# Optimization experiments

Measured on AMD Instinct MI355X. Metric: run time of the kernel, lower is better.

Reference implementation:

```python
import jax, jax.numpy as jnp
import numpy as np

NUM_NODES = 100000
DIM_E = 64
NEG_SLOPE = 0.01  # F.leaky_relu default


def setup_inputs() -> dict:
    key = jax.random.key(0)
    ks = jax.random.split(key, 8)
    edge_index = jax.random.randint(ks[0], (2, 1000000), 0, NUM_NODES, dtype=jnp.int64)
    # xavier_normal for id_embedding: std = sqrt(2/(fan_in+fan_out))
    std_emb = float(np.sqrt(2.0 / (NUM_NODES + DIM_E)))
    id_embedding = jax.random.normal(ks[1], (NUM_NODES, DIM_E), dtype=jnp.float32) * std_emb
    std_w = float(np.sqrt(2.0 / (DIM_E + DIM_E)))  # glorot for GCN lin weight [out, in]
    W1 = jax.random.normal(ks[2], (DIM_E, DIM_E), dtype=jnp.float32) * std_w
    W2 = jax.random.normal(ks[3], (DIM_E, DIM_E), dtype=jnp.float32) * std_w
    W3 = jax.random.normal(ks[4], (DIM_E, DIM_E), dtype=jnp.float32) * std_w
    b1 = jnp.zeros((DIM_E,), dtype=jnp.float32)
    b2 = jnp.zeros((DIM_E,), dtype=jnp.float32)
    b3 = jnp.zeros((DIM_E,), dtype=jnp.float32)
    return {"edge_index": edge_index, "id_embedding": id_embedding,
            "W1": W1, "b1": b1, "W2": W2, "b2": b2, "W3": W3, "b3": b3}


def _build_graph(edge_index, n):
    # symmetrize (as done in RealGCN.forward) then add self loops (PyG GCNConv default)
    ei = jnp.concatenate([edge_index, edge_index[::-1]], axis=1)
    loops = jnp.arange(n, dtype=ei.dtype)
    row = jnp.concatenate([ei[0], loops])  # source
    col = jnp.concatenate([ei[1], loops])  # destination
    deg = jax.ops.segment_sum(jnp.ones_like(col, dtype=jnp.float32), col, num_segments=n)
    dinv = jnp.where(deg > 0, jax.lax.rsqrt(deg), 0.0)
    norm = dinv[row] * dinv[col]  # [E_total]
    return row, col, norm


def _gcn_conv(x, row, col, norm, W, b, n):
    h = x @ W.T                                   # [N, D] linear transform
    msg = h[row] * norm[:, None]                  # gather + normalize
    out = jax.ops.segment_sum(msg, col, num_segments=n)  # scatter-add
    return out + b


def reference(edge_index, id_embedding, W1, b1, W2, b2, W3, b3):
    n = id_embedding.shape[0]
    row, col, norm = _build_graph(edge_index, n)
    # has_norm: L2-normalize rows (F.normalize, eps=1e-12)
    nrm = jnp.linalg.norm(id_embedding, axis=1, keepdims=True)
    x = id_embedding / jnp.maximum(nrm, 1e-12)
    x1 = jax.nn.leaky_relu(_gcn_conv(x, row, col, norm, W1, b1, n), NEG_SLOPE)
    x2 = jax.nn.leaky_relu(_gcn_conv(x1, row, col, norm, W2, b2, n), NEG_SLOPE)
    x3 = _gcn_conv(x1, row, col, norm, W3, b3, n)  # note: layer 3 has no activation
    return x + x1 + x2 + x3
```

## Files before the change

### kernel.cpp

```cpp
#include <hip/hip_runtime.h>
#include <math.h>

#define DIM 64
#define NEG_SLOPE 0.01f

typedef unsigned short bfraw;
typedef unsigned int uint32;

__device__ __forceinline__ bfraw f2bf(float f) {
    unsigned int u = __float_as_uint(f);
    unsigned int r = (u + 0x7FFFu + ((u >> 16) & 1u)) >> 16;
    return (bfraw)r;
}
__device__ __forceinline__ float bflo(uint32 u) { return __uint_as_float(u << 16); }
__device__ __forceinline__ float bfhi(uint32 u) { return __uint_as_float(u & 0xFFFF0000u); }
__device__ __forceinline__ uint32 pack2(float lo, float hi) {
    return (uint32)f2bf(lo) | ((uint32)f2bf(hi) << 16);
}

#define EPW 4096

__global__ __launch_bounds__(256) void k_bin(const int* __restrict__ ei, int E,
                                             uint32* __restrict__ stage,
                                             int* __restrict__ bcur, int shift, int sbits,
                                             int capS) {
    __shared__ int hist[256];
    __shared__ int cur[256];
    int t = threadIdx.x;
    hist[t] = 0;
    __syncthreads();
    int e0 = blockIdx.x * EPW;
    int e1 = e0 + EPW < E ? e0 + EPW : E;
    uint32 lmask = (1u << shift) - 1u;
    for (int e = e0 + t; e < e1; e += 256) {
        int u = ei[e], v = ei[E + e];
        atomicAdd(&hist[u >> shift], 1);
        atomicAdd(&hist[v >> shift], 1);
    }
    __syncthreads();
    cur[t] = hist[t] > 0 ? (t * capS + atomicAdd(&bcur[t * 16], hist[t])) : 0;
    __syncthreads();
    for (int e = e0 + t; e < e1; e += 256) {
        int u = ei[e], v = ei[E + e];
        int s1 = atomicAdd(&cur[v >> shift], 1);
        stage[s1] = (((uint32)v & lmask) << sbits) | (uint32)u;
        int s2 = atomicAdd(&cur[u >> shift], 1);
        stage[s2] = (((uint32)u & lmask) << sbits) | (uint32)v;
    }
}

__global__ __launch_bounds__(256) void k_bucket(const uint32* __restrict__ stage,
                                                const int* __restrict__ bcur,
                                                int* __restrict__ offsets,
                                                int* __restrict__ oend,
                                                int* __restrict__ adj,
                                                float* __restrict__ dinv,
                                                int n, int shift, int sbits,
                                                int capS, int capA) {
    __shared__ int deg[2048];
    __shared__ int scan[256];
    int t = threadIdx.x;
    int span  = 1 << shift;
    int node0 = blockIdx.x << shift;
    int cnt = n - node0 < span ? n - node0 : span;
    uint32 smask = (1u << sbits) - 1u;
    for (int i = t; i < cnt; i += 256) deg[i] = 0;
    __syncthreads();
    int jbeg = blockIdx.x * capS;
    int jend = jbeg + bcur[blockIdx.x * 16];
    for (int j = jbeg + t; j < jend; j += 256)
        atomicAdd(&deg[stage[j] >> sbits], 1);
    __syncthreads();
    int per  = span >> 8;
    int base = t * per;
    int s = 0;
    for (int k = 0; k < per; k++) { int i = base + k; if (i < cnt) s += deg[i] + 1; }
    scan[t] = s;
    __syncthreads();
    for (int off = 1; off < 256; off <<= 1) {
        int v = (t >= off) ? scan[t - off] : 0;
        __syncthreads();
        scan[t] += v;
        __syncthreads();
    }
    int run = blockIdx.x * capA + scan[t] - s;
    for (int k = 0; k < per; k++) {
        int i = base + k;
        if (i < cnt) {
            int d = deg[i];
            offsets[node0 + i] = run;
            oend[node0 + i]    = run + 1 + d;
            dinv[node0 + i] = rsqrtf(1.0f + (float)d);
            adj[run] = node0 + i;
            deg[i] = run + 1;
            run += d + 1;
        }
    }
    __syncthreads();
    for (int j = jbeg + t; j < jend; j += 256) {
        uint32 r = stage[j];
        int slot = atomicAdd(&deg[r >> sbits], 1);
        adj[slot] = (int)(r & smask);
    }
}

__global__ void k_normalize(const float* __restrict__ x, const float* __restrict__ dinv,
                            bfraw* __restrict__ xnb, bfraw* __restrict__ xnw, int n) {
    int row  = (blockIdx.x * blockDim.x + threadIdx.x) >> 6;
    int lane = threadIdx.x & 63;
    if (row >= n) return;
    float v = x[row * DIM + lane];
    float s = v * v;
    #pragma unroll
    for (int off = 32; off; off >>= 1) s += __shfl_xor(s, off);
    float scale = 1.0f / fmaxf(sqrtf(s), 1e-12f);
    float xv = v * scale;
    xnb[row * DIM + lane] = f2bf(xv);
    xnw[row * DIM + lane] = f2bf(xv * dinv[row]);
}

#define ACC8(p) { a0 += bflo(p.x); a1 += bfhi(p.x); a2 += bflo(p.y); a3 += bfhi(p.y); \
                  a4 += bflo(p.z); a5 += bfhi(p.z); a6 += bflo(p.w); a7 += bfhi(p.w); }

__global__ void k_gather(const int* __restrict__ adj, const int* __restrict__ offsets,
                         const int* __restrict__ oend,
                         const float* __restrict__ dinv,
                         const bfraw* __restrict__ srcw,
                         bfraw* __restrict__ dstb, int n) {
    int w    = (blockIdx.x * blockDim.x + threadIdx.x) >> 6;
    int lane = threadIdx.x & 63;
    if (w >= n) return;
    int oct = lane >> 3;
    int ol  = lane & 7;
    int beg = offsets[w], end = oend[w];
    float dd = dinv[w];
    const uint4* rows = (const uint4*)srcw;
    float a0 = 0.f, a1 = 0.f, a2 = 0.f, a3 = 0.f;
    float a4 = 0.f, a5 = 0.f, a6 = 0.f, a7 = 0.f;
    int j = beg;
    for (; j + 32 <= end; j += 32) {
        int s0 = adj[j + oct];
        int s1 = adj[j + 8 + oct];
        int s2 = adj[j + 16 + oct];
        int s3 = adj[j + 24 + oct];
        uint4 p0 = rows[(size_t)s0 * 8 + ol];
        uint4 p1 = rows[(size_t)s1 * 8 + ol];
        uint4 p2 = rows[(size_t)s2 * 8 + ol];
        uint4 p3 = rows[(size_t)s3 * 8 + ol];
        ACC8(p0) ACC8(p1) ACC8(p2) ACC8(p3)
    }
    if (j + 16 <= end) {
        int s0 = adj[j + oct];
        int s1 = adj[j + 8 + oct];
        uint4 p0 = rows[(size_t)s0 * 8 + ol];
        uint4 p1 = rows[(size_t)s1 * 8 + ol];
        ACC8(p0) ACC8(p1)
        j += 16;
    }
    if (j + 8 <= end) {
        int s0 = adj[j + oct];
        uint4 p0 = rows[(size_t)s0 * 8 + ol];
        ACC8(p0)
        j += 8;
    }
    int rem = end - j;
    if (oct < rem) {
        int s0 = adj[j + oct];
        uint4 p0 = rows[(size_t)s0 * 8 + ol];
        ACC8(p0)
    }
    a0 += __shfl_xor(a0, 8); a0 += __shfl_xor(a0, 16); a0 += __shfl_xor(a0, 32);
    a1 += __shfl_xor(a1, 8); a1 += __shfl_xor(a1, 16); a1 += __shfl_xor(a1, 32);
    a2 += __shfl_xor(a2, 8); a2 += __shfl_xor(a2, 16); a2 += __shfl_xor(a2, 32);
    a3 += __shfl_xor(a3, 8); a3 += __shfl_xor(a3, 16); a3 += __shfl_xor(a3, 32);
    a4 += __shfl_xor(a4, 8); a4 += __shfl_xor(a4, 16); a4 += __shfl_xor(a4, 32);
    a5 += __shfl_xor(a5, 8); a5 += __shfl_xor(a5, 16); a5 += __shfl_xor(a5, 32);
    a6 += __shfl_xor(a6, 8); a6 += __shfl_xor(a6, 16); a6 += __shfl_xor(a6, 32);
    a7 += __shfl_xor(a7, 8); a7 += __shfl_xor(a7, 16); a7 += __shfl_xor(a7, 32);
    if (lane < 8) {
        uint4 o;
        o.x = pack2(dd * a0, dd * a1);
        o.y = pack2(dd * a2, dd * a3);
        o.z = pack2(dd * a4, dd * a5);
        o.w = pack2(dd * a6, dd * a7);
        ((uint4*)(dstb + (size_t)w * DIM))[ol] = o;
    }
}


__global__ __launch_bounds__(256) void k_linear_rt(
    const bfraw* __restrict__ inb, const float* __restrict__ W,
    const float* __restrict__ b, const float* __restrict__ dinv,
    bfraw* __restrict__ outb, bfraw* __restrict__ outw, int n)
{
    __shared__ float  sIn[64][65];
    __shared__ uint32 sWp[64][32];
    int tid = threadIdx.x;
    int r0  = blockIdx.x * 64;
    #pragma unroll
    for (int i = 0; i < 8; i++) {
        int idx = tid + i * 256;
        int k = idx & 63, cp = idx >> 6;
        sWp[k][cp] = (uint32)f2bf(W[(2 * cp) * DIM + k]) |
                     ((uint32)f2bf(W[(2 * cp + 1) * DIM + k]) << 16);
    }
    int limu = ((n - r0 < 64 ? n - r0 : 64) * DIM) >> 1;
    const uint32* inu = (const uint32*)(inb + (size_t)r0 * DIM);
    for (int idx = tid; idx < limu; idx += 256) {
        uint32 u = inu[idx];
        int r = idx >> 5, c = (idx & 31) * 2;
        sIn[r][c] = bflo(u); sIn[r][c + 1] = bfhi(u);
    }
    __syncthreads();

    int ri = (tid >> 4) << 2;
    int ci = (tid & 15) << 2;
    int cp = ci >> 1;
    float acc[4][4];
    #pragma unroll
    for (int j = 0; j < 4; j++) {
        float bj = b[ci + j];
        #pragma unroll
        for (int i = 0; i < 4; i++) acc[i][j] = bj;
    }
    #pragma unroll 2
    for (int k4 = 0; k4 < 16; k4++) {
        int k = k4 * 4;
        float4 A0 = *(const float4*)&sIn[ri + 0][k];
        float4 A1 = *(const float4*)&sIn[ri + 1][k];
        float4 A2 = *(const float4*)&sIn[ri + 2][k];
        float4 A3 = *(const float4*)&sIn[ri + 3][k];
        #pragma unroll
        for (int kk = 0; kk < 4; kk++) {
            uint2 uw = *(const uint2*)&sWp[k + kk][cp];
            float w0 = bflo(uw.x), w1 = bfhi(uw.x);
            float w2 = bflo(uw.y), w3 = bfhi(uw.y);
            float a0 = kk == 0 ? A0.x : kk == 1 ? A0.y : kk == 2 ? A0.z : A0.w;
            float a1 = kk == 0 ? A1.x : kk == 1 ? A1.y : kk == 2 ? A1.z : A1.w;
            float a2 = kk == 0 ? A2.x : kk == 1 ? A2.y : kk == 2 ? A2.z : A2.w;
            float a3 = kk == 0 ? A3.x : kk == 1 ? A3.y : kk == 2 ? A3.z : A3.w;
            acc[0][0] = fmaf(a0, w0, acc[0][0]); acc[0][1] = fmaf(a0, w1, acc[0][1]);
            acc[0][2] = fmaf(a0, w2, acc[0][2]); acc[0][3] = fmaf(a0, w3, acc[0][3]);
            acc[1][0] = fmaf(a1, w0, acc[1][0]); acc[1][1] = fmaf(a1, w1, acc[1][1]);
            acc[1][2] = fmaf(a1, w2, acc[1][2]); acc[1][3] = fmaf(a1, w3, acc[1][3]);
            acc[2][0] = fmaf(a2, w0, acc[2][0]); acc[2][1] = fmaf(a2, w1, acc[2][1]);
            acc[2][2] = fmaf(a2, w2, acc[2][2]); acc[2][3] = fmaf(a2, w3, acc[2][3]);
            acc[3][0] = fmaf(a3, w0, acc[3][0]); acc[3][1] = fmaf(a3, w1, acc[3][1]);
            acc[3][2] = fmaf(a3, w2, acc[3][2]); acc[3][3] = fmaf(a3, w3, acc[3][3]);
        }
    }
    #pragma unroll
    for (int i = 0; i < 4; i++) {
        int r = r0 + ri + i;
        if (r >= n) break;
        float dd = dinv[r];
        float e0 = acc[i][0] > 0.f ? acc[i][0] : NEG_SLOPE * acc[i][0];
        float e1 = acc[i][1] > 0.f ? acc[i][1] : NEG_SLOPE * acc[i][1];
        float e2 = acc[i][2] > 0.f ? acc[i][2] : NEG_SLOPE * acc[i][2];
        float e3 = acc[i][3] > 0.f ? acc[i][3] : NEG_SLOPE * acc[i][3];
        ushort4 ob;
        ob.x = f2bf(e0); ob.y = f2bf(e1); ob.z = f2bf(e2); ob.w = f2bf(e3);
        *(ushort4*)&outb[(size_t)r * DIM + ci] = ob;
        ushort4 ow;
        ow.x = f2bf(e0 * dd); ow.y = f2bf(e1 * dd);
        ow.z = f2bf(e2 * dd); ow.w = f2bf(e3 * dd);
        *(ushort4*)&outw[(size_t)r * DIM + ci] = ow;
    }
}

__global__ __launch_bounds__(256) void k_final_rt(
    const bfraw* __restrict__ aggb, const bfraw* __restrict__ xnb,
    const bfraw* __restrict__ x1b,
    const float* __restrict__ W2, const float* __restrict__ b2,
    const float* __restrict__ W3, const float* __restrict__ b3,
    float* __restrict__ out, int n)
{
    __shared__ float  sIn[64][65];
    __shared__ uint32 sW2p[64][32];
    __shared__ uint32 sW3p[64][32];
    int tid = threadIdx.x;
    int r0  = blockIdx.x * 64;
    #pragma unroll
    for (int i = 0; i < 8; i++) {
        int idx = tid + i * 256;
        int k = idx & 63, cp = idx >> 6;
        sW2p[k][cp] = (uint32)f2bf(W2[(2 * cp) * DIM + k]) |
                      ((uint32)f2bf(W2[(2 * cp + 1) * DIM + k]) << 16);
        sW3p[k][cp] = (uint32)f2bf(W3[(2 * cp) * DIM + k]) |
                      ((uint32)f2bf(W3[(2 * cp + 1) * DIM + k]) << 16);
    }
    int limu = ((n - r0 < 64 ? n - r0 : 64) * DIM) >> 1;
    const uint32* inu = (const uint32*)(aggb + (size_t)r0 * DIM);
    for (int idx = tid; idx < limu; idx += 256) {
        uint32 u = inu[idx];
        int r = idx >> 5, c = (idx & 31) * 2;
        sIn[r][c] = bflo(u); sIn[r][c + 1] = bfhi(u);
    }
    __syncthreads();

    int ri = (tid >> 4) << 2;
    int ci = (tid & 15) << 2;
    int cp = ci >> 1;
    float acc2[4][4], acc3[4][4];
    #pragma unroll
    for (int j = 0; j < 4; j++) {
        float bj2 = b2[ci + j], bj3 = b3[ci + j];
        #pragma unroll
        for (int i = 0; i < 4; i++) { acc2[i][j] = bj2; acc3[i][j] = bj3; }
    }
    #pragma unroll 2
    for (int k4 = 0; k4 < 16; k4++) {
        int k = k4 * 4;
        float4 A0 = *(const float4*)&sIn[ri + 0][k];
        float4 A1 = *(const float4*)&sIn[ri + 1][k];
        float4 A2 = *(const float4*)&sIn[ri + 2][k];
        float4 A3 = *(const float4*)&sIn[ri + 3][k];
        #pragma unroll
        for (int kk = 0; kk < 4; kk++) {
            uint2 u2 = *(const uint2*)&sW2p[k + kk][cp];
            uint2 u3 = *(const uint2*)&sW3p[k + kk][cp];
            float a0 = kk == 0 ? A0.x : kk == 1 ? A0.y : kk == 2 ? A0.z : A0.w;
            float a1 = kk == 0 ? A1.x : kk == 1 ? A1.y : kk == 2 ? A1.z : A1.w;
            float a2 = kk == 0 ? A2.x : kk == 1 ? A2.y : kk == 2 ? A2.z : A2.w;
            float a3 = kk == 0 ? A3.x : kk == 1 ? A3.y : kk == 2 ? A3.z : A3.w;
            float u0 = bflo(u2.x), u1 = bfhi(u2.x), u2c = bflo(u2.y), u3c = bfhi(u2.y);
            float v0 = bflo(u3.x), v1 = bfhi(u3.x), v2c = bflo(u3.y), v3c = bfhi(u3.y);
            acc2[0][0] = fmaf(a0, u0, acc2[0][0]); acc2[0][1] = fmaf(a0, u1, acc2[0][1]);
            acc2[0][2] = fmaf(a0, u2c, acc2[0][2]); acc2[0][3] = fmaf(a0, u3c, acc2[0][3]);
            acc2[1][0] = fmaf(a1, u0, acc2[1][0]); acc2[1][1] = fmaf(a1, u1, acc2[1][1]);
            acc2[1][2] = fmaf(a1, u2c, acc2[1][2]); acc2[1][3] = fmaf(a1, u3c, acc2[1][3]);
            acc2[2][0] = fmaf(a2, u0, acc2[2][0]); acc2[2][1] = fmaf(a2, u1, acc2[2][1]);
            acc2[2][2] = fmaf(a2, u2c, acc2[2][2]); acc2[2][3] = fmaf(a2, u3c, acc2[2][3]);
            acc2[3][0] = fmaf(a3, u0, acc2[3][0]); acc2[3][1] = fmaf(a3, u1, acc2[3][1]);
            acc2[3][2] = fmaf(a3, u2c, acc2[3][2]); acc2[3][3] = fmaf(a3, u3c, acc2[3][3]);
            acc3[0][0] = fmaf(a0, v0, acc3[0][0]); acc3[0][1] = fmaf(a0, v1, acc3[0][1]);
            acc3[0][2] = fmaf(a0, v2c, acc3[0][2]); acc3[0][3] = fmaf(a0, v3c, acc3[0][3]);
            acc3[1][0] = fmaf(a1, v0, acc3[1][0]); acc3[1][1] = fmaf(a1, v1, acc3[1][1]);
            acc3[1][2] = fmaf(a1, v2c, acc3[1][2]); acc3[1][3] = fmaf(a1, v3c, acc3[1][3]);
            acc3[2][0] = fmaf(a2, v0, acc3[2][0]); acc3[2][1] = fmaf(a2, v1, acc3[2][1]);
            acc3[2][2] = fmaf(a2, v2c, acc3[2][2]); acc3[2][3] = fmaf(a2, v3c, acc3[2][3]);
            acc3[3][0] = fmaf(a3, v0, acc3[3][0]); acc3[3][1] = fmaf(a3, v1, acc3[3][1]);
            acc3[3][2] = fmaf(a3, v2c, acc3[3][2]); acc3[3][3] = fmaf(a3, v3c, acc3[3][3]);
        }
    }
    #pragma unroll
    for (int i = 0; i < 4; i++) {
        int r = r0 + ri + i;
        if (r >= n) break;
        size_t base = (size_t)r * DIM + ci;
        uint2 uxn = *(const uint2*)&xnb[base];
        uint2 ux1 = *(const uint2*)&x1b[base];
        float4 o;
        float e0 = acc2[i][0] > 0.f ? acc2[i][0] : NEG_SLOPE * acc2[i][0];
        float e1 = acc2[i][1] > 0.f ? acc2[i][1] : NEG_SLOPE * acc2[i][1];
        float e2 = acc2[i][2] > 0.f ? acc2[i][2] : NEG_SLOPE * acc2[i][2];
        float e3 = acc2[i][3] > 0.f ? acc2[i][3] : NEG_SLOPE * acc2[i][3];
        o.x = bflo(uxn.x) + bflo(ux1.x) + e0 + acc3[i][0];
        o.y = bfhi(uxn.x) + bfhi(ux1.x) + e1 + acc3[i][1];
        o.z = bflo(uxn.y) + bflo(ux1.y) + e2 + acc3[i][2];
        o.w = bfhi(uxn.y) + bfhi(ux1.y) + e3 + acc3[i][3];
        *(float4*)&out[base] = o;
    }
}


extern "C" void kernel_launch(void* const* d_in, const int* in_sizes, int n_in,
                              void* d_out, int out_size, void* d_ws, size_t ws_size,
                              hipStream_t stream) {
    const int*   ei  = (const int*)d_in[0];
    const float* emb = (const float*)d_in[1];
    const float* W1  = (const float*)d_in[2];
    const float* b1  = (const float*)d_in[3];
    const float* W2  = (const float*)d_in[4];
    const float* b2  = (const float*)d_in[5];
    const float* W3  = (const float*)d_in[6];
    const float* b3  = (const float*)d_in[7];
    float* out = (float*)d_out;

    int E = in_sizes[0] / 2;
    int n = in_sizes[1] / DIM;
    size_t nD = (size_t)n * DIM;

    int shift = 9;
    while ((((size_t)n + ((size_t)1 << shift) - 1) >> shift) > 256) shift++;
    int nbuckets = (int)(((size_t)n + ((size_t)1 << shift) - 1) >> shift);
    int sbits = 32 - shift;
    int span  = 1 << shift;

    int capS = (int)(2 * (size_t)E / nbuckets + (2 * (size_t)E) / (4 * (size_t)nbuckets) + 2048);
    if ((size_t)nbuckets * capS > nD / 2) capS = (int)((nD / 2) / nbuckets);
    int capA = capS + span;

    size_t np   = ((size_t)n + 1023) & ~1023ull;
    size_t adjn = ((size_t)nbuckets * capA + 31) & ~31ull;
    int*   bcur    = (int*)d_ws;
    int*   offsets = bcur + 4096;
    int*   oendA   = offsets + np;
    float* dinv    = (float*)(oendA + np);
    bfraw* aggb    = (bfraw*)(dinv + np);
    int*   adj     = (int*)(aggb + nD);
    bfraw* xnw     = (bfraw*)(adj + adjn);
    bfraw* x1w     = xnw + nD;
    bfraw* xnb     = x1w + nD;
    bfraw* x1b     = xnb + nD;
    uint32* stage  = (uint32*)aggb;

    const int B = 256;

    hipMemsetAsync(bcur, 0, 4096 * sizeof(int), stream);
    k_bin   <<<(E + EPW - 1) / EPW, B, 0, stream>>>(ei, E, stage, bcur, shift, sbits, capS);
    k_bucket<<<nbuckets, B, 0, stream>>>(stage, bcur, offsets, oendA, adj, dinv,
                                         n, shift, sbits, capS, capA);

    k_normalize<<<(n + 3) / 4, B, 0, stream>>>(emb, dinv, xnb, xnw, n);

    k_gather   <<<(n + 3) / 4, B, 0, stream>>>(adj, offsets, oendA, dinv, xnw, aggb, n);
    k_linear_rt<<<(n + 63) / 64, B, 0, stream>>>(aggb, W1, b1, dinv, x1b, x1w, n);

    k_gather   <<<(n + 3) / 4, B, 0, stream>>>(adj, offsets, oendA, dinv, x1w, aggb, n);
    k_final_rt <<<(n + 63) / 64, B, 0, stream>>>(aggb, xnb, x1b, W2, b2, W3, b3, out, n);
}
```

Baseline: 219.2 us.

## Fuse neighbor gather into linear and final transform kernels

The separate gather kernels are merged into the per-64-row linear kernels. Each wave aggregates 16 destination rows straight into shared memory in fp32, so the bf16 aggregation buffer is no longer written and re-read and two launches go away. The workspace is re-laid out to drop that buffer, with the binning stage now aliasing the xnb buffer and a larger capacity limit. In exchange, each block now has only 4 waves doing latency-bound gathers, with 16 sequential rows per wave, which lowers memory-level parallelism and occupancy compared with one wave per row.

```diff
diff --git a/kernel.cpp b/kernel.cpp
--- a/kernel.cpp
+++ b/kernel.cpp
@@ -14,9 +14,6 @@
 }
 __device__ __forceinline__ float bflo(uint32 u) { return __uint_as_float(u << 16); }
 __device__ __forceinline__ float bfhi(uint32 u) { return __uint_as_float(u & 0xFFFF0000u); }
-__device__ __forceinline__ uint32 pack2(float lo, float hi) {
-    return (uint32)f2bf(lo) | ((uint32)f2bf(hi) << 16);
-}
 
 #define EPW 4096
 
@@ -122,75 +119,57 @@
 #define ACC8(p) { a0 += bflo(p.x); a1 += bfhi(p.x); a2 += bflo(p.y); a3 += bfhi(p.y); \
                   a4 += bflo(p.z); a5 += bfhi(p.z); a6 += bflo(p.w); a7 += bfhi(p.w); }
 
-__global__ void k_gather(const int* __restrict__ adj, const int* __restrict__ offsets,
-                         const int* __restrict__ oend,
-                         const float* __restrict__ dinv,
-                         const bfraw* __restrict__ srcw,
-                         bfraw* __restrict__ dstb, int n) {
-    int w    = (blockIdx.x * blockDim.x + threadIdx.x) >> 6;
-    int lane = threadIdx.x & 63;
-    if (w >= n) return;
-    int oct = lane >> 3;
-    int ol  = lane & 7;
-    int beg = offsets[w], end = oend[w];
-    float dd = dinv[w];
-    const uint4* rows = (const uint4*)srcw;
-    float a0 = 0.f, a1 = 0.f, a2 = 0.f, a3 = 0.f;
-    float a4 = 0.f, a5 = 0.f, a6 = 0.f, a7 = 0.f;
-    int j = beg;
-    for (; j + 32 <= end; j += 32) {
-        int s0 = adj[j + oct];
-        int s1 = adj[j + 8 + oct];
-        int s2 = adj[j + 16 + oct];
-        int s3 = adj[j + 24 + oct];
-        uint4 p0 = rows[(size_t)s0 * 8 + ol];
-        uint4 p1 = rows[(size_t)s1 * 8 + ol];
-        uint4 p2 = rows[(size_t)s2 * 8 + ol];
-        uint4 p3 = rows[(size_t)s3 * 8 + ol];
-        ACC8(p0) ACC8(p1) ACC8(p2) ACC8(p3)
-    }
-    if (j + 16 <= end) {
-        int s0 = adj[j + oct];
-        int s1 = adj[j + 8 + oct];
-        uint4 p0 = rows[(size_t)s0 * 8 + ol];
-        uint4 p1 = rows[(size_t)s1 * 8 + ol];
-        ACC8(p0) ACC8(p1)
-        j += 16;
-    }
-    if (j + 8 <= end) {
-        int s0 = adj[j + oct];
-        uint4 p0 = rows[(size_t)s0 * 8 + ol];
-        ACC8(p0)
-        j += 8;
-    }
-    int rem = end - j;
-    if (oct < rem) {
-        int s0 = adj[j + oct];
-        uint4 p0 = rows[(size_t)s0 * 8 + ol];
-        ACC8(p0)
-    }
-    a0 += __shfl_xor(a0, 8); a0 += __shfl_xor(a0, 16); a0 += __shfl_xor(a0, 32);
-    a1 += __shfl_xor(a1, 8); a1 += __shfl_xor(a1, 16); a1 += __shfl_xor(a1, 32);
-    a2 += __shfl_xor(a2, 8); a2 += __shfl_xor(a2, 16); a2 += __shfl_xor(a2, 32);
-    a3 += __shfl_xor(a3, 8); a3 += __shfl_xor(a3, 16); a3 += __shfl_xor(a3, 32);
-    a4 += __shfl_xor(a4, 8); a4 += __shfl_xor(a4, 16); a4 += __shfl_xor(a4, 32);
-    a5 += __shfl_xor(a5, 8); a5 += __shfl_xor(a5, 16); a5 += __shfl_xor(a5, 32);
-    a6 += __shfl_xor(a6, 8); a6 += __shfl_xor(a6, 16); a6 += __shfl_xor(a6, 32);
+#define GATHER_BODY(adj, beg, end, rows, oct, ol)                                  \
+    float a0 = 0.f, a1 = 0.f, a2 = 0.f, a3 = 0.f;                                  \
+    float a4 = 0.f, a5 = 0.f, a6 = 0.f, a7 = 0.f;                                  \
+    {                                                                              \
+        int j = beg;                                                               \
+        for (; j + 32 <= end; j += 32) {                                           \
+            int s0 = adj[j + oct];                                                 \
+            int s1 = adj[j + 8 + oct];                                             \
+            int s2 = adj[j + 16 + oct];                                            \
+            int s3 = adj[j + 24 + oct];                                            \
+            uint4 p0 = rows[(size_t)s0 * 8 + ol];                                  \
+            uint4 p1 = rows[(size_t)s1 * 8 + ol];                                  \
+            uint4 p2 = rows[(size_t)s2 * 8 + ol];                                  \
+            uint4 p3 = rows[(size_t)s3 * 8 + ol];                                  \
+            ACC8(p0) ACC8(p1) ACC8(p2) ACC8(p3)                                    \
+        }                                                                          \
+        if (j + 16 <= end) {                                                       \
+            int s0 = adj[j + oct];                                                 \
+            int s1 = adj[j + 8 + oct];                                             \
+            uint4 p0 = rows[(size_t)s0 * 8 + ol];                                  \
+            uint4 p1 = rows[(size_t)s1 * 8 + ol];                                  \
+            ACC8(p0) ACC8(p1)                                                      \
+            j += 16;                                                               \
+        }                                                                          \
+        if (j + 8 <= end) {                                                        \
+            int s0 = adj[j + oct];                                                 \
+            uint4 p0 = rows[(size_t)s0 * 8 + ol];                                  \
+            ACC8(p0)                                                               \
+            j += 8;                                                                \
+        }                                                                          \
+        int rem = end - j;                                                         \
+        if (oct < rem) {                                                           \
+            int s0 = adj[j + oct];                                                 \
+            uint4 p0 = rows[(size_t)s0 * 8 + ol];                                  \
+            ACC8(p0)                                                               \
+        }                                                                          \
+    }                                                                              \
+    a0 += __shfl_xor(a0, 8); a0 += __shfl_xor(a0, 16); a0 += __shfl_xor(a0, 32);   \
+    a1 += __shfl_xor(a1, 8); a1 += __shfl_xor(a1, 16); a1 += __shfl_xor(a1, 32);   \
+    a2 += __shfl_xor(a2, 8); a2 += __shfl_xor(a2, 16); a2 += __shfl_xor(a2, 32);   \
+    a3 += __shfl_xor(a3, 8); a3 += __shfl_xor(a3, 16); a3 += __shfl_xor(a3, 32);   \
+    a4 += __shfl_xor(a4, 8); a4 += __shfl_xor(a4, 16); a4 += __shfl_xor(a4, 32);   \
+    a5 += __shfl_xor(a5, 8); a5 += __shfl_xor(a5, 16); a5 += __shfl_xor(a5, 32);   \
+    a6 += __shfl_xor(a6, 8); a6 += __shfl_xor(a6, 16); a6 += __shfl_xor(a6, 32);   \
     a7 += __shfl_xor(a7, 8); a7 += __shfl_xor(a7, 16); a7 += __shfl_xor(a7, 32);
-    if (lane < 8) {
-        uint4 o;
-        o.x = pack2(dd * a0, dd * a1);
-        o.y = pack2(dd * a2, dd * a3);
-        o.z = pack2(dd * a4, dd * a5);
-        o.w = pack2(dd * a6, dd * a7);
-        ((uint4*)(dstb + (size_t)w * DIM))[ol] = o;
-    }
-}
-
-
-__global__ __launch_bounds__(256) void k_linear_rt(
-    const bfraw* __restrict__ inb, const float* __restrict__ W,
-    const float* __restrict__ b, const float* __restrict__ dinv,
+
+__global__ __launch_bounds__(256) void k_gather_lin(
+    const int* __restrict__ adj, const int* __restrict__ offsets,
+    const int* __restrict__ oend, const float* __restrict__ dinv,
+    const bfraw* __restrict__ srcw,
+    const float* __restrict__ W, const float* __restrict__ b,
     bfraw* __restrict__ outb, bfraw* __restrict__ outw, int n)
 {
     __shared__ float  sIn[64][65];
@@ -204,12 +183,26 @@
         sWp[k][cp] = (uint32)f2bf(W[(2 * cp) * DIM + k]) |
                      ((uint32)f2bf(W[(2 * cp + 1) * DIM + k]) << 16);
     }
-    int limu = ((n - r0 < 64 ? n - r0 : 64) * DIM) >> 1;
-    const uint32* inu = (const uint32*)(inb + (size_t)r0 * DIM);
-    for (int idx = tid; idx < limu; idx += 256) {
-        uint32 u = inu[idx];
-        int r = idx >> 5, c = (idx & 31) * 2;
-        sIn[r][c] = bflo(u); sIn[r][c + 1] = bfhi(u);
+    int wv = tid >> 6, lane = tid & 63;
+    int oct = lane >> 3, ol = lane & 7;
+    const uint4* rows = (const uint4*)srcw;
+    for (int t = 0; t < 16; t++) {
+        int r = wv * 16 + t;
+        int w = r0 + r;
+        if (w < n) {
+            int beg = offsets[w], end = oend[w];
+            GATHER_BODY(adj, beg, end, rows, oct, ol)
+            float dd = dinv[w];
+            if (lane < 8) {
+                sIn[r][8*ol+0] = dd*a0; sIn[r][8*ol+1] = dd*a1;
+                sIn[r][8*ol+2] = dd*a2; sIn[r][8*ol+3] = dd*a3;
+                sIn[r][8*ol+4] = dd*a4; sIn[r][8*ol+5] = dd*a5;
+                sIn[r][8*ol+6] = dd*a6; sIn[r][8*ol+7] = dd*a7;
+            }
+        } else if (lane < 8) {
+            #pragma unroll
+            for (int i = 0; i < 8; i++) sIn[r][8*ol+i] = 0.f;
+        }
     }
     __syncthreads();
 
@@ -268,9 +261,11 @@
     }
 }
 
-__global__ __launch_bounds__(256) void k_final_rt(
-    const bfraw* __restrict__ aggb, const bfraw* __restrict__ xnb,
-    const bfraw* __restrict__ x1b,
+__global__ __launch_bounds__(256) void k_gather_fin(
+    const int* __restrict__ adj, const int* __restrict__ offsets,
+    const int* __restrict__ oend, const float* __restrict__ dinv,
+    const bfraw* __restrict__ srcw,
+    const bfraw* __restrict__ xnb, const bfraw* __restrict__ x1b,
     const float* __restrict__ W2, const float* __restrict__ b2,
     const float* __restrict__ W3, const float* __restrict__ b3,
     float* __restrict__ out, int n)
@@ -289,12 +284,26 @@
         sW3p[k][cp] = (uint32)f2bf(W3[(2 * cp) * DIM + k]) |
                       ((uint32)f2bf(W3[(2 * cp + 1) * DIM + k]) << 16);
     }
-    int limu = ((n - r0 < 64 ? n - r0 : 64) * DIM) >> 1;
-    const uint32* inu = (const uint32*)(aggb + (size_t)r0 * DIM);
-    for (int idx = tid; idx < limu; idx += 256) {
-        uint32 u = inu[idx];
-        int r = idx >> 5, c = (idx & 31) * 2;
-        sIn[r][c] = bflo(u); sIn[r][c + 1] = bfhi(u);
+    int wv = tid >> 6, lane = tid & 63;
+    int oct = lane >> 3, ol = lane & 7;
+    const uint4* rows = (const uint4*)srcw;
+    for (int t = 0; t < 16; t++) {
+        int r = wv * 16 + t;
+        int w = r0 + r;
+        if (w < n) {
+            int beg = offsets[w], end = oend[w];
+            GATHER_BODY(adj, beg, end, rows, oct, ol)
+            float dd = dinv[w];
+            if (lane < 8) {
+                sIn[r][8*ol+0] = dd*a0; sIn[r][8*ol+1] = dd*a1;
+                sIn[r][8*ol+2] = dd*a2; sIn[r][8*ol+3] = dd*a3;
+                sIn[r][8*ol+4] = dd*a4; sIn[r][8*ol+5] = dd*a5;
+                sIn[r][8*ol+6] = dd*a6; sIn[r][8*ol+7] = dd*a7;
+            }
+        } else if (lane < 8) {
+            #pragma unroll
+            for (int i = 0; i < 8; i++) sIn[r][8*ol+i] = 0.f;
+        }
     }
     __syncthreads();
 
@@ -388,7 +397,7 @@
     int span  = 1 << shift;
 
     int capS = (int)(2 * (size_t)E / nbuckets + (2 * (size_t)E) / (4 * (size_t)nbuckets) + 2048);
-    if ((size_t)nbuckets * capS > nD / 2) capS = (int)((nD / 2) / nbuckets);
+    if ((size_t)nbuckets * capS > nD) capS = (int)(nD / nbuckets);
     int capA = capS + span;
 
     size_t np   = ((size_t)n + 1023) & ~1023ull;
@@ -397,13 +406,12 @@
     int*   offsets = bcur + 4096;
     int*   oendA   = offsets + np;
     float* dinv    = (float*)(oendA + np);
-    bfraw* aggb    = (bfraw*)(dinv + np);
-    int*   adj     = (int*)(aggb + nD);
+    int*   adj     = (int*)(dinv + np);
     bfraw* xnw     = (bfraw*)(adj + adjn);
     bfraw* x1w     = xnw + nD;
     bfraw* xnb     = x1w + nD;
     bfraw* x1b     = xnb + nD;
-    uint32* stage  = (uint32*)aggb;
+    uint32* stage  = (uint32*)xnb;
 
     const int B = 256;
 
@@ -414,9 +422,9 @@
 
     k_normalize<<<(n + 3) / 4, B, 0, stream>>>(emb, dinv, xnb, xnw, n);
 
-    k_gather   <<<(n + 3) / 4, B, 0, stream>>>(adj, offsets, oendA, dinv, xnw, aggb, n);
-    k_linear_rt<<<(n + 63) / 64, B, 0, stream>>>(aggb, W1, b1, dinv, x1b, x1w, n);
-
-    k_gather   <<<(n + 3) / 4, B, 0, stream>>>(adj, offsets, oendA, dinv, x1w, aggb, n);
-    k_final_rt <<<(n + 63) / 64, B, 0, stream>>>(aggb, xnb, x1b, W2, b2, W3, b3, out, n);
-}
+    k_gather_lin<<<(n + 63) / 64, B, 0, stream>>>(adj, offsets, oendA, dinv, xnw,
+                                                  W1, b1, x1b, x1w, n);
+
+    k_gather_fin<<<(n + 63) / 64, B, 0, stream>>>(adj, offsets, oendA, dinv, x1w,
+                                                  xnb, x1b, W2, b2, W3, b3, out, n);
+}
```

Measured after the change: 270.0 us. 23.2% more time.

## Drop unscaled bf16 copies and use finer edge buckets

Applied to the files above, without the earlier changes.

Stops writing separate unscaled bf16 copies of the normalized input and layer-1 output, and reconstructs them in the final kernel by dividing the dinv-scaled copies by dinv. This cuts global writes and workspace. Also raises the maximum bucket count to 1024, with a smaller initial shift, so the bucketing kernel launches more, smaller blocks. The reconstruction adds a small rounding difference from the scaled bf16 values.

```diff
diff --git a/kernel.cpp b/kernel.cpp
--- a/kernel.cpp
+++ b/kernel.cpp
@@ -3,6 +3,7 @@
 
 #define DIM 64
 #define NEG_SLOPE 0.01f
+#define NBMAX 1024
 
 typedef unsigned short bfraw;
 typedef unsigned int uint32;
@@ -23,11 +24,11 @@
 __global__ __launch_bounds__(256) void k_bin(const int* __restrict__ ei, int E,
                                              uint32* __restrict__ stage,
                                              int* __restrict__ bcur, int shift, int sbits,
-                                             int capS) {
-    __shared__ int hist[256];
-    __shared__ int cur[256];
+                                             int capS, int nbuckets) {
+    __shared__ int hist[NBMAX];
+    __shared__ int cur[NBMAX];
     int t = threadIdx.x;
-    hist[t] = 0;
+    for (int i = t; i < nbuckets; i += 256) hist[i] = 0;
     __syncthreads();
     int e0 = blockIdx.x * EPW;
     int e1 = e0 + EPW < E ? e0 + EPW : E;
@@ -38,7 +39,8 @@
         atomicAdd(&hist[v >> shift], 1);
     }
     __syncthreads();
-    cur[t] = hist[t] > 0 ? (t * capS + atomicAdd(&bcur[t * 16], hist[t])) : 0;
+    for (int i = t; i < nbuckets; i += 256)
+        cur[i] = hist[i] > 0 ? (i * capS + atomicAdd(&bcur[i * 16], hist[i])) : 0;
     __syncthreads();
     for (int e = e0 + t; e < e1; e += 256) {
         int u = ei[e], v = ei[E + e];
@@ -72,6 +74,7 @@
         atomicAdd(&deg[stage[j] >> sbits], 1);
     __syncthreads();
     int per  = span >> 8;
+    if (per < 1) per = 1;
     int base = t * per;
     int s = 0;
     for (int k = 0; k < per; k++) { int i = base + k; if (i < cnt) s += deg[i] + 1; }
@@ -105,7 +108,7 @@
 }
 
 __global__ void k_normalize(const float* __restrict__ x, const float* __restrict__ dinv,
-                            bfraw* __restrict__ xnb, bfraw* __restrict__ xnw, int n) {
+                            bfraw* __restrict__ xnw, int n) {
     int row  = (blockIdx.x * blockDim.x + threadIdx.x) >> 6;
     int lane = threadIdx.x & 63;
     if (row >= n) return;
@@ -114,9 +117,7 @@
     #pragma unroll
     for (int off = 32; off; off >>= 1) s += __shfl_xor(s, off);
     float scale = 1.0f / fmaxf(sqrtf(s), 1e-12f);
-    float xv = v * scale;
-    xnb[row * DIM + lane] = f2bf(xv);
-    xnw[row * DIM + lane] = f2bf(xv * dinv[row]);
+    xnw[row * DIM + lane] = f2bf(v * scale * dinv[row]);
 }
 
 #define ACC8(p) { a0 += bflo(p.x); a1 += bfhi(p.x); a2 += bflo(p.y); a3 += bfhi(p.y); \
@@ -187,11 +188,10 @@
     }
 }
 
-
 __global__ __launch_bounds__(256) void k_linear_rt(
     const bfraw* __restrict__ inb, const float* __restrict__ W,
     const float* __restrict__ b, const float* __restrict__ dinv,
-    bfraw* __restrict__ outb, bfraw* __restrict__ outw, int n)
+    bfraw* __restrict__ outw, int n)
 {
     __shared__ float  sIn[64][65];
     __shared__ uint32 sWp[64][32];
@@ -258,9 +258,6 @@
         float e1 = acc[i][1] > 0.f ? acc[i][1] : NEG_SLOPE * acc[i][1];
         float e2 = acc[i][2] > 0.f ? acc[i][2] : NEG_SLOPE * acc[i][2];
         float e3 = acc[i][3] > 0.f ? acc[i][3] : NEG_SLOPE * acc[i][3];
-        ushort4 ob;
-        ob.x = f2bf(e0); ob.y = f2bf(e1); ob.z = f2bf(e2); ob.w = f2bf(e3);
-        *(ushort4*)&outb[(size_t)r * DIM + ci] = ob;
         ushort4 ow;
         ow.x = f2bf(e0 * dd); ow.y = f2bf(e1 * dd);
         ow.z = f2bf(e2 * dd); ow.w = f2bf(e3 * dd);
@@ -269,8 +266,8 @@
 }
 
 __global__ __launch_bounds__(256) void k_final_rt(
-    const bfraw* __restrict__ aggb, const bfraw* __restrict__ xnb,
-    const bfraw* __restrict__ x1b,
+    const bfraw* __restrict__ aggb, const bfraw* __restrict__ xnw,
+    const bfraw* __restrict__ x1w, const float* __restrict__ dinv,
     const float* __restrict__ W2, const float* __restrict__ b2,
     const float* __restrict__ W3, const float* __restrict__ b3,
     float* __restrict__ out, int n)
@@ -348,17 +345,18 @@
         int r = r0 + ri + i;
         if (r >= n) break;
         size_t base = (size_t)r * DIM + ci;
-        uint2 uxn = *(const uint2*)&xnb[base];
-        uint2 ux1 = *(const uint2*)&x1b[base];
+        float rdd = 1.0f / dinv[r];
+        uint2 uxn = *(const uint2*)&xnw[base];
+        uint2 ux1 = *(const uint2*)&x1w[base];
         float4 o;
         float e0 = acc2[i][0] > 0.f ? acc2[i][0] : NEG_SLOPE * acc2[i][0];
         float e1 = acc2[i][1] > 0.f ? acc2[i][1] : NEG_SLOPE * acc2[i][1];
         float e2 = acc2[i][2] > 0.f ? acc2[i][2] : NEG_SLOPE * acc2[i][2];
         float e3 = acc2[i][3] > 0.f ? acc2[i][3] : NEG_SLOPE * acc2[i][3];
-        o.x = bflo(uxn.x) + bflo(ux1.x) + e0 + acc3[i][0];
-        o.y = bfhi(uxn.x) + bfhi(ux1.x) + e1 + acc3[i][1];
-        o.z = bflo(uxn.y) + bflo(ux1.y) + e2 + acc3[i][2];
-        o.w = bfhi(uxn.y) + bfhi(ux1.y) + e3 + acc3[i][3];
+        o.x = (bflo(uxn.x) + bflo(ux1.x)) * rdd + e0 + acc3[i][0];
+        o.y = (bfhi(uxn.x) + bfhi(ux1.x)) * rdd + e1 + acc3[i][1];
+        o.z = (bflo(uxn.y) + bflo(ux1.y)) * rdd + e2 + acc3[i][2];
+        o.w = (bfhi(uxn.y) + bfhi(ux1.y)) * rdd + e3 + acc3[i][3];
         *(float4*)&out[base] = o;
     }
 }
@@ -381,42 +379,41 @@
     int n = in_sizes[1] / DIM;
     size_t nD = (size_t)n * DIM;
 
-    int shift = 9;
-    while ((((size_t)n + ((size_t)1 << shift) - 1) >> shift) > 256) shift++;
+    int shift = 8;
+    while ((((size_t)n + ((size_t)1 << shift) - 1) >> shift) > NBMAX) shift++;
     int nbuckets = (int)(((size_t)n + ((size_t)1 << shift) - 1) >> shift);
     int sbits = 32 - shift;
     int span  = 1 << shift;
 
     int capS = (int)(2 * (size_t)E / nbuckets + (2 * (size_t)E) / (4 * (size_t)nbuckets) + 2048);
-    if ((size_t)nbuckets * capS > nD / 2) capS = (int)((nD / 2) / nbuckets);
+    if ((size_t)nbuckets * capS > nD) capS = (int)(nD / nbuckets);
     int capA = capS + span;
 
     size_t np   = ((size_t)n + 1023) & ~1023ull;
     size_t adjn = ((size_t)nbuckets * capA + 31) & ~31ull;
     int*   bcur    = (int*)d_ws;
-    int*   offsets = bcur + 4096;
+    int*   offsets = bcur + NBMAX * 16;
     int*   oendA   = offsets + np;
     float* dinv    = (float*)(oendA + np);
     bfraw* aggb    = (bfraw*)(dinv + np);
-    int*   adj     = (int*)(aggb + nD);
-    bfraw* xnw     = (bfraw*)(adj + adjn);
+    bfraw* xnw     = aggb + nD;
     bfraw* x1w     = xnw + nD;
-    bfraw* xnb     = x1w + nD;
-    bfraw* x1b     = xnb + nD;
+    int*   adj     = (int*)(x1w + nD);
     uint32* stage  = (uint32*)aggb;
 
     const int B = 256;
 
-    hipMemsetAsync(bcur, 0, 4096 * sizeof(int), stream);
-    k_bin   <<<(E + EPW - 1) / EPW, B, 0, stream>>>(ei, E, stage, bcur, shift, sbits, capS);
+    hipMemsetAsync(bcur, 0, NBMAX * 16 * sizeof(int), stream);
+    k_bin   <<<(E + EPW - 1) / EPW, B, 0, stream>>>(ei, E, stage, bcur, shift, sbits,
+                                                    capS, nbuckets);
     k_bucket<<<nbuckets, B, 0, stream>>>(stage, bcur, offsets, oendA, adj, dinv,
                                          n, shift, sbits, capS, capA);
 
-    k_normalize<<<(n + 3) / 4, B, 0, stream>>>(emb, dinv, xnb, xnw, n);
+    k_normalize<<<(n + 3) / 4, B, 0, stream>>>(emb, dinv, xnw, n);
 
     k_gather   <<<(n + 3) / 4, B, 0, stream>>>(adj, offsets, oendA, dinv, xnw, aggb, n);
-    k_linear_rt<<<(n + 63) / 64, B, 0, stream>>>(aggb, W1, b1, dinv, x1b, x1w, n);
+    k_linear_rt<<<(n + 63) / 64, B, 0, stream>>>(aggb, W1, b1, dinv, x1w, n);
 
     k_gather   <<<(n + 3) / 4, B, 0, stream>>>(adj, offsets, oendA, dinv, x1w, aggb, n);
-    k_final_rt <<<(n + 63) / 64, B, 0, stream>>>(aggb, xnb, x1b, W2, b2, W3, b3, out, n);
-}
+    k_final_rt <<<(n + 63) / 64, B, 0, stream>>>(aggb, xnw, x1w, dinv, W2, b2, W3, b3, out, n);
+}
```

Measured after the change: 211.2 us, median of 2. 3.7% less time.
